# Performance work log

Hardware: AMD Instinct MI355X
Metric: run time of the kernel (lower is better)

The kernel has to match this reference:

```python
import jax, jax.numpy as jnp
import numpy as np

GAMMA = 0.3
R_PERCENT = 0.2
LAMBDA_PENALTY = 0.5
EPS = 1e-06

B_SZ, N_HEADS, K_FULL = 16, 32, 32768
K_IMG = 16384


def _zscore(x):
    mu = x.mean(axis=-1, keepdims=True)
    std = jnp.sqrt(((x - mu) ** 2).mean(axis=-1, keepdims=True))  # unbiased=False
    return (x - mu) / (std + EPS)


def _topk_binary(scores, k):
    # scores: [B,H] -> binary mask [B,H]; only strictly-positive topk values count
    vals, idx = jax.lax.top_k(scores, k)
    b = jnp.arange(scores.shape[0])[:, None]
    return jnp.zeros_like(scores).at[b, idx].set((vals > 0).astype(scores.dtype))


def setup_inputs() -> dict:
    key = jax.random.key(0)
    k1, k2, k3, k4, k5 = jax.random.split(key, 5)
    attn_logits_last = jax.random.normal(k1, (B_SZ, N_HEADS, K_FULL), dtype=jnp.float32)
    # exactly K_IMG image tokens per row (alternating pattern -> strided gather)
    image_mask = jnp.tile((jnp.arange(K_FULL) % 2 == 0).astype(jnp.int32)[None, :], (B_SZ, 1))
    feat_C = jax.random.normal(k2, (B_SZ, K_IMG), dtype=jnp.float32)
    feat_A = jax.random.normal(k3, (B_SZ, K_IMG), dtype=jnp.float32)
    feat_D = jax.random.normal(k4, (B_SZ, K_IMG), dtype=jnp.float32)
    feat_B = jax.random.normal(k5, (B_SZ, K_IMG), dtype=jnp.float32)
    return {"attn_logits_last": attn_logits_last, "image_mask": image_mask,
            "feat_C": feat_C, "feat_A": feat_A, "feat_D": feat_D, "feat_B": feat_B}


def reference(attn_logits_last, image_mask, feat_C, feat_A, feat_D, feat_B):
    B, H, K_full = attn_logits_last.shape
    K_img = feat_C.shape[1]

    # --- compute_rf ---
    C_t = jax.nn.relu(_zscore(feat_C))
    A_t = jax.nn.sigmoid(_zscore(feat_A))
    D_t = jax.nn.sigmoid(_zscore(feat_D))
    B_t = jax.nn.sigmoid(_zscore(feat_B))
    denom = jnp.maximum(1.0 + LAMBDA_PENALTY * (D_t + B_t), EPS)
    rf = jnp.maximum(C_t * A_t / denom, 0.0)  # [B,K_img]

    # --- align: positions of image tokens (exactly K_img ones per row) ---
    idx = jax.vmap(lambda m: jnp.nonzero(m, size=K_img)[0])(image_mask)  # [B,K_img]

    # --- image-normalized attention ---
    probs_full = jax.nn.softmax(attn_logits_last, axis=-1)
    mask_f = image_mask[:, None, :].astype(attn_logits_last.dtype)  # [B,1,K_full]
    probs_img = probs_full * mask_f
    probs_img_norm = probs_img / jnp.maximum(probs_img.sum(axis=-1, keepdims=True), EPS)
    attn_img_norm = jnp.take_along_axis(probs_img_norm, idx[:, None, :], axis=-1)  # [B,H,K_img]

    # --- dynamic head roles ---
    low_rf = jnp.maximum(1.0 - rf, 0.0)
    s_pos = (attn_img_norm * rf[:, None, :]).sum(axis=-1)   # [B,H]
    s_neg = (attn_img_norm * low_rf[:, None, :]).sum(axis=-1)
    k_heads = min(max(1, int(np.ceil(R_PERCENT * H))), H)
    m_pos = _topk_binary(s_pos, k_heads)
    neg_scores = jnp.where(m_pos > 0, -jnp.inf, s_neg)
    m_neg = _topk_binary(neg_scores, k_heads) * (m_pos == 0).astype(s_pos.dtype)

    # --- delta and scatter back to full logits ---
    delta_img = GAMMA * (m_pos[:, :, None] * rf[:, None, :]
                         - m_neg[:, :, None] * low_rf[:, None, :])  # [B,H,K_img]
    delta_full = jax.vmap(
        lambda d, i: jnp.zeros((H, K_full), attn_logits_last.dtype).at[:, i].set(d)
    )(delta_img, idx)
    delta_full = delta_full * mask_f
    return attn_logits_last + delta_full
```

## Files before the change

kernel.cpp:

```cpp
#include <hip/hip_runtime.h>
#include <math.h>

#define GAMMA 0.3f
#define EPS 1e-6f
#define B_SZ 16
#define NH 32
#define KF 32768
#define KI 16384
#define KHEADS 7

constexpr int OFF_MU    = 0;
constexpr int OFF_SD    = 64;
constexpr int OFF_RAWS  = 128;
constexpr int OFF_RAWP  = 640;
constexpr int OFF_RAWN  = 1152;
constexpr int IOFF_BSUM = 1664;
constexpr int OFF_RFF   = 4096;


__global__ __launch_bounds__(256) void k_stats_cnt(const float* __restrict__ fC,
        const float* __restrict__ fA, const float* __restrict__ fD,
        const float* __restrict__ fB, const int* __restrict__ mask,
        float* __restrict__ ws) {
    __shared__ double r1[256], r2[256];
    __shared__ int sred[256];
    int bid = blockIdx.x, t = threadIdx.x;
    if (bid < 64) {
        int b = bid >> 2, f = bid & 3;
        const float* src;
        if (f == 0) src = fC; else if (f == 1) src = fA; else if (f == 2) src = fD; else src = fB;
        src += (size_t)b * KI;
        double s = 0.0, s2 = 0.0;
        for (int i = t; i < KI / 4; i += 256) {
            float4 v = ((const float4*)src)[i];
            s  += (double)v.x + (double)v.y + (double)v.z + (double)v.w;
            s2 += (double)v.x * v.x + (double)v.y * v.y + (double)v.z * v.z + (double)v.w * v.w;
        }
        r1[t] = s; r2[t] = s2; __syncthreads();
        for (int off = 128; off > 0; off >>= 1) {
            if (t < off) { r1[t] += r1[t + off]; r2[t] += r2[t + off]; }
            __syncthreads();
        }
        if (t == 0) {
            double mu  = r1[0] * (1.0 / KI);
            double var = fmax(r2[0] * (1.0 / KI) - mu * mu, 0.0);
            ws[OFF_MU + bid] = (float)mu;
            ws[OFF_SD + bid] = (float)(sqrt(var) + (double)EPS);
        }
    } else {
        int cblk = bid - 64;
        if (cblk < 6) ws[OFF_RAWS + cblk * 256 + t] = 0.f;
        const int* mrow = mask + (size_t)cblk * 2048;
        int4 m0 = *(const int4*)(mrow + t * 8);
        int4 m1 = *(const int4*)(mrow + t * 8 + 4);
        int cnt = (m0.x != 0) + (m0.y != 0) + (m0.z != 0) + (m0.w != 0)
                + (m1.x != 0) + (m1.y != 0) + (m1.z != 0) + (m1.w != 0);
        sred[t] = cnt; __syncthreads();
        for (int off = 128; off > 0; off >>= 1) {
            if (t < off) sred[t] += sred[t + off];
            __syncthreads();
        }
        if (t == 0) ((int*)ws)[IOFF_BSUM + cblk] = sred[0];
    }
}

__global__ __launch_bounds__(256) void k_rf_expand(const float* __restrict__ fC,
        const float* __restrict__ fA, const float* __restrict__ fD,
        const float* __restrict__ fB, const int* __restrict__ mask,
        float* __restrict__ ws) {
    __shared__ int sc[256];
    __shared__ float rfbuf[2048];
    int blk = blockIdx.x, t = threadIdx.x;
    int b = blk >> 4, c = blk & 15;
    const int* bsum = (const int*)ws + IOFF_BSUM;
    int boff = 0;
    for (int i = 0; i < c; ++i) boff += bsum[(b << 4) + i];
    const int* mrow = mask + (size_t)blk * 2048;
    int4 m0 = *(const int4*)(mrow + t * 8);
    int4 m1 = *(const int4*)(mrow + t * 8 + 4);
    int mv[8] = {m0.x, m0.y, m0.z, m0.w, m1.x, m1.y, m1.z, m1.w};
    int cnt = 0;
    #pragma unroll
    for (int j = 0; j < 8; ++j) cnt += (mv[j] != 0);
    sc[t] = cnt; __syncthreads();
    for (int off = 1; off < 256; off <<= 1) {
        int v = (t >= off) ? sc[t - off] : 0;
        __syncthreads();
        sc[t] += v;
        __syncthreads();
    }
    int total = sc[255];
    int rloc = sc[t] - cnt;
    float mu0 = ws[OFF_MU + b * 4 + 0], sd0 = ws[OFF_SD + b * 4 + 0];
    float mu1 = ws[OFF_MU + b * 4 + 1], sd1 = ws[OFF_SD + b * 4 + 1];
    float mu2 = ws[OFF_MU + b * 4 + 2], sd2 = ws[OFF_SD + b * 4 + 2];
    float mu3 = ws[OFF_MU + b * 4 + 3], sd3 = ws[OFF_SD + b * 4 + 3];
    for (int j = t; j < total; j += 256) {
        size_t idx = (size_t)b * KI + boff + j;
        float Ct = fmaxf((fC[idx] - mu0) / sd0, 0.f);
        float At = 1.f / (1.f + __expf(-((fA[idx] - mu1) / sd1)));
        float Dt = 1.f / (1.f + __expf(-((fD[idx] - mu2) / sd2)));
        float Bt = 1.f / (1.f + __expf(-((fB[idx] - mu3) / sd3)));
        float denom = fmaxf(1.f + 0.5f * (Dt + Bt), EPS);
        rfbuf[j] = fmaxf(Ct * At / denom, 0.f);
    }
    __syncthreads();
    float vr[8];
    #pragma unroll
    for (int j = 0; j < 8; ++j) {
        if (mv[j]) { vr[j] = rfbuf[rloc]; ++rloc; }
        else       { vr[j] = -1.f; }
    }
    float* rff = ws + OFF_RFF + (size_t)blk * 2048 + t * 8;
    *(float4*)(rff)     = *(float4*)(vr);
    *(float4*)(rff + 4) = *(float4*)(vr + 4);
}

__global__ __launch_bounds__(256) void k_scores(const float* __restrict__ attn,
                                                float* __restrict__ ws) {
    int g = blockIdx.x, t = threadIdx.x;
    int bh = g >> 1, half = g & 1;
    int b = bh >> 5;
    const float* xr  = attn + ((size_t)bh << 15) + ((size_t)half << 14);
    const float* rff = ws + OFF_RFF + ((size_t)b << 15) + ((size_t)half << 14);
    float S = 0.f, P = 0.f, N = 0.f;
    #pragma unroll 4
    for (int i = 0; i < 16; ++i) {
        int k = (i * 256 + t) * 4;
        float4 xs = *(const float4*)(xr + k);
        float4 rv = *(const float4*)(rff + k);
        float xa[4] = {xs.x, xs.y, xs.z, xs.w};
        float va[4] = {rv.x, rv.y, rv.z, rv.w};
        #pragma unroll
        for (int j = 0; j < 4; ++j) {
            float e = __expf(xa[j]);
            bool on = va[j] >= 0.f;
            float rfv  = fmaxf(va[j], 0.f);
            float lrfv = on ? fmaxf(1.f - va[j], 0.f) : 0.f;
            S += on ? e : 0.f;
            P = fmaf(e, rfv, P);
            N = fmaf(e, lrfv, N);
        }
    }
    __shared__ float rs[256], rp[256], rn[256];
    rs[t] = S; rp[t] = P; rn[t] = N;
    __syncthreads();
    for (int off = 128; off > 0; off >>= 1) {
        if (t < off) { rs[t] += rs[t + off]; rp[t] += rp[t + off]; rn[t] += rn[t + off]; }
        __syncthreads();
    }
    if (t == 0) {
        atomicAdd(&ws[OFF_RAWS + bh], rs[0]);
        atomicAdd(&ws[OFF_RAWP + bh], rp[0]);
        atomicAdd(&ws[OFF_RAWN + bh], rn[0]);
    }
}

__global__ __launch_bounds__(256) void k_out(const float* __restrict__ attn,
        const float* __restrict__ ws, float* __restrict__ out) {
    unsigned int t = threadIdx.x;
    unsigned int flat = blockIdx.x * 2048 + t * 8;
    unsigned int bh = flat >> 15;
    unsigned int b  = bh >> 5;
    unsigned int h  = bh & 31;

    __shared__ float ssp[NH], snv[NH];
    __shared__ int smp[NH];
    __shared__ float s_gp, s_gn;
    if (t < NH) {
        float S0 = ws[OFF_RAWS + b * NH + t];
        ssp[t] = ws[OFF_RAWP + b * NH + t] / S0;
        snv[t] = ws[OFF_RAWN + b * NH + t] / S0;
    }
    __syncthreads();
    if (t < NH) {
        float sp = ssp[t];
        int cnt = 0;
        for (int j = 0; j < NH; ++j) { float o = ssp[j]; cnt += (o > sp) || (o == sp && j < (int)t); }
        smp[t] = (cnt < KHEADS) && (sp > 0.f);
    }
    __syncthreads();
    if (t < NH && smp[t]) snv[t] = -INFINITY;
    __syncthreads();
    if (t == 0) {
        float gp = 0.f, gn = 0.f;
        if (smp[h]) gp = GAMMA;
        else {
            float nv = snv[h];
            int cnt = 0;
            for (int j = 0; j < NH; ++j) { float o = snv[j]; cnt += (o > nv) || (o == nv && j < (int)h); }
            if ((cnt < KHEADS) && (nv > 0.f)) gn = GAMMA;
        }
        s_gp = gp; s_gn = gn;
    }
    __syncthreads();

    float gp = s_gp, gn = s_gn;
    const float* rff = ws + OFF_RFF + ((size_t)b << 15);
    unsigned int k = flat & (KF - 1);
    #pragma unroll
    for (int half8 = 0; half8 < 2; ++half8) {
        unsigned int f2 = flat + half8 * 4, k2 = k + half8 * 4;
        float4 xs = *(const float4*)(attn + f2);
        float4 rv = *(const float4*)(rff + k2);
        float va[4] = {rv.x, rv.y, rv.z, rv.w};
        float xa[4] = {xs.x, xs.y, xs.z, xs.w};
        float oa[4];
        #pragma unroll
        for (int j = 0; j < 4; ++j) {
            bool on = va[j] >= 0.f;
            float rfv  = fmaxf(va[j], 0.f);
            float lrfv = on ? fmaxf(1.f - va[j], 0.f) : 0.f;
            oa[j] = xa[j] + gp * rfv - gn * lrfv;
        }
        float4 o = {oa[0], oa[1], oa[2], oa[3]};
        *(float4*)(out + f2) = o;
    }
}

extern "C" void kernel_launch(void* const* d_in, const int* in_sizes, int n_in,
                              void* d_out, int out_size, void* d_ws, size_t ws_size,
                              hipStream_t stream) {
    const float* attn = (const float*)d_in[0];
    const int*   mask = (const int*)d_in[1];
    const float* fC   = (const float*)d_in[2];
    const float* fA   = (const float*)d_in[3];
    const float* fD   = (const float*)d_in[4];
    const float* fB   = (const float*)d_in[5];
    float* out = (float*)d_out;
    float* ws = (float*)d_ws;

    k_stats_cnt<<<320, 256, 0, stream>>>(fC, fA, fD, fB, mask, ws);
    k_rf_expand<<<256, 256, 0, stream>>>(fC, fA, fD, fB, mask, ws);
    k_scores   <<<1024, 256, 0, stream>>>(attn, ws);
    k_out      <<<B_SZ * NH * KF / 2048, 256, 0, stream>>>(attn, ws, out);
}
```

Measured before the change: 149.9 us.

## Fuse scores and output pass with register-held logits and per-batch spin barrier

Merges the stats, count and rf-expansion kernels into one pre-kernel: each block recomputes the feature statistics and its own prefix of the mask. The score and output kernels become a single kernel that keeps its 16 float4 logits in registers. A per-batch atomic counter with a spin-wait holds blocks until all 64 blocks of that batch have added their head sums. This removes the second global read of the attention logits and two launches. The spin barrier assumes all 64 blocks of a batch are resident at once, which is a deadlock risk, and the pre-kernel repeats the reduction work in every block.

```diff
diff --git a/kernel.cpp b/kernel.cpp
--- a/kernel.cpp
+++ b/kernel.cpp
@@ -9,27 +9,33 @@
 #define KI 16384
 #define KHEADS 7
 
-constexpr int OFF_MU    = 0;
-constexpr int OFF_SD    = 64;
-constexpr int OFF_RAWS  = 128;
-constexpr int OFF_RAWP  = 640;
-constexpr int OFF_RAWN  = 1152;
-constexpr int IOFF_BSUM = 1664;
-constexpr int OFF_RFF   = 4096;
-
-
-__global__ __launch_bounds__(256) void k_stats_cnt(const float* __restrict__ fC,
+constexpr int OFF_RAWS = 0;
+constexpr int OFF_RAWP = 512;
+constexpr int OFF_RAWN = 1024;
+constexpr int IOFF_ARR = 1536;
+constexpr int OFF_RFF  = 4096;
+
+
+__global__ __launch_bounds__(256) void k_pre(const float* __restrict__ fC,
         const float* __restrict__ fA, const float* __restrict__ fD,
         const float* __restrict__ fB, const int* __restrict__ mask,
         float* __restrict__ ws) {
     __shared__ double r1[256], r2[256];
-    __shared__ int sred[256];
-    int bid = blockIdx.x, t = threadIdx.x;
-    if (bid < 64) {
-        int b = bid >> 2, f = bid & 3;
-        const float* src;
-        if (f == 0) src = fC; else if (f == 1) src = fA; else if (f == 2) src = fD; else src = fB;
-        src += (size_t)b * KI;
+    __shared__ float s_mu[4], s_sd[4];
+    __shared__ int sc[256];
+    __shared__ float rfbuf[2048];
+    int blk = blockIdx.x, t = threadIdx.x;
+    int b = blk >> 4, c = blk & 15;
+
+    if (blk == 0) {
+        for (int i = t; i < 1536; i += 256) ws[OFF_RAWS + i] = 0.f;
+        if (t < 16) ((int*)ws)[IOFF_ARR + t * 32] = 0;
+    }
+
+    const float* feats[4] = {fC, fA, fD, fB};
+    #pragma unroll 1
+    for (int f = 0; f < 4; ++f) {
+        const float* src = feats[f] + (size_t)b * KI;
         double s = 0.0, s2 = 0.0;
         for (int i = t; i < KI / 4; i += 256) {
             float4 v = ((const float4*)src)[i];
@@ -44,38 +50,27 @@
         if (t == 0) {
             double mu  = r1[0] * (1.0 / KI);
             double var = fmax(r2[0] * (1.0 / KI) - mu * mu, 0.0);
-            ws[OFF_MU + bid] = (float)mu;
-            ws[OFF_SD + bid] = (float)(sqrt(var) + (double)EPS);
-        }
-    } else {
-        int cblk = bid - 64;
-        if (cblk < 6) ws[OFF_RAWS + cblk * 256 + t] = 0.f;
-        const int* mrow = mask + (size_t)cblk * 2048;
-        int4 m0 = *(const int4*)(mrow + t * 8);
-        int4 m1 = *(const int4*)(mrow + t * 8 + 4);
-        int cnt = (m0.x != 0) + (m0.y != 0) + (m0.z != 0) + (m0.w != 0)
-                + (m1.x != 0) + (m1.y != 0) + (m1.z != 0) + (m1.w != 0);
-        sred[t] = cnt; __syncthreads();
-        for (int off = 128; off > 0; off >>= 1) {
-            if (t < off) sred[t] += sred[t + off];
-            __syncthreads();
-        }
-        if (t == 0) ((int*)ws)[IOFF_BSUM + cblk] = sred[0];
-    }
-}
-
-__global__ __launch_bounds__(256) void k_rf_expand(const float* __restrict__ fC,
-        const float* __restrict__ fA, const float* __restrict__ fD,
-        const float* __restrict__ fB, const int* __restrict__ mask,
-        float* __restrict__ ws) {
-    __shared__ int sc[256];
-    __shared__ float rfbuf[2048];
-    int blk = blockIdx.x, t = threadIdx.x;
-    int b = blk >> 4, c = blk & 15;
-    const int* bsum = (const int*)ws + IOFF_BSUM;
-    int boff = 0;
-    for (int i = 0; i < c; ++i) boff += bsum[(b << 4) + i];
-    const int* mrow = mask + (size_t)blk * 2048;
+            s_mu[f] = (float)mu;
+            s_sd[f] = (float)(sqrt(var) + (double)EPS);
+        }
+        __syncthreads();
+    }
+
+    const int* mrowb = mask + (size_t)b * KF;
+    int pre = 0;
+    for (int i = t; i < c * 512; i += 256) {
+        int4 m = ((const int4*)mrowb)[i];
+        pre += (m.x != 0) + (m.y != 0) + (m.z != 0) + (m.w != 0);
+    }
+    sc[t] = pre; __syncthreads();
+    for (int off = 128; off > 0; off >>= 1) {
+        if (t < off) sc[t] += sc[t + off];
+        __syncthreads();
+    }
+    int boff = sc[0];
+    __syncthreads();
+
+    const int* mrow = mrowb + c * 2048;
     int4 m0 = *(const int4*)(mrow + t * 8);
     int4 m1 = *(const int4*)(mrow + t * 8 + 4);
     int mv[8] = {m0.x, m0.y, m0.z, m0.w, m1.x, m1.y, m1.z, m1.w};
@@ -91,10 +86,9 @@
     }
     int total = sc[255];
     int rloc = sc[t] - cnt;
-    float mu0 = ws[OFF_MU + b * 4 + 0], sd0 = ws[OFF_SD + b * 4 + 0];
-    float mu1 = ws[OFF_MU + b * 4 + 1], sd1 = ws[OFF_SD + b * 4 + 1];
-    float mu2 = ws[OFF_MU + b * 4 + 2], sd2 = ws[OFF_SD + b * 4 + 2];
-    float mu3 = ws[OFF_MU + b * 4 + 3], sd3 = ws[OFF_SD + b * 4 + 3];
+
+    float mu0 = s_mu[0], sd0 = s_sd[0], mu1 = s_mu[1], sd1 = s_sd[1];
+    float mu2 = s_mu[2], sd2 = s_sd[2], mu3 = s_mu[3], sd3 = s_sd[3];
     for (int j = t; j < total; j += 256) {
         size_t idx = (size_t)b * KI + boff + j;
         float Ct = fmaxf((fC[idx] - mu0) / sd0, 0.f);
@@ -116,19 +110,22 @@
     *(float4*)(rff + 4) = *(float4*)(vr + 4);
 }
 
-__global__ __launch_bounds__(256) void k_scores(const float* __restrict__ attn,
-                                                float* __restrict__ ws) {
+__global__ __launch_bounds__(256, 4) void k_main(const float* __restrict__ attn,
+        float* __restrict__ ws, float* __restrict__ out) {
     int g = blockIdx.x, t = threadIdx.x;
     int bh = g >> 1, half = g & 1;
-    int b = bh >> 5;
+    int b = bh >> 5, h = bh & 31;
     const float* xr  = attn + ((size_t)bh << 15) + ((size_t)half << 14);
     const float* rff = ws + OFF_RFF + ((size_t)b << 15) + ((size_t)half << 14);
+
+    float4 r[16];
     float S = 0.f, P = 0.f, N = 0.f;
-    #pragma unroll 4
+    #pragma unroll
     for (int i = 0; i < 16; ++i) {
         int k = (i * 256 + t) * 4;
         float4 xs = *(const float4*)(xr + k);
         float4 rv = *(const float4*)(rff + k);
+        r[i] = xs;
         float xa[4] = {xs.x, xs.y, xs.z, xs.w};
         float va[4] = {rv.x, rv.y, rv.z, rv.w};
         #pragma unroll
@@ -149,35 +146,35 @@
         if (t < off) { rs[t] += rs[t + off]; rp[t] += rp[t + off]; rn[t] += rn[t + off]; }
         __syncthreads();
     }
+
+    int* arr = (int*)ws + IOFF_ARR + b * 32;
     if (t == 0) {
         atomicAdd(&ws[OFF_RAWS + bh], rs[0]);
         atomicAdd(&ws[OFF_RAWP + bh], rp[0]);
         atomicAdd(&ws[OFF_RAWN + bh], rn[0]);
-    }
-}
-
-__global__ __launch_bounds__(256) void k_out(const float* __restrict__ attn,
-        const float* __restrict__ ws, float* __restrict__ out) {
-    unsigned int t = threadIdx.x;
-    unsigned int flat = blockIdx.x * 2048 + t * 8;
-    unsigned int bh = flat >> 15;
-    unsigned int b  = bh >> 5;
-    unsigned int h  = bh & 31;
+        __threadfence();
+        atomicAdd(arr, 1);
+        while (__hip_atomic_load(arr, __ATOMIC_RELAXED, __HIP_MEMORY_SCOPE_AGENT) < 64)
+            __builtin_amdgcn_s_sleep(2);
+    }
+    __syncthreads();
 
     __shared__ float ssp[NH], snv[NH];
     __shared__ int smp[NH];
     __shared__ float s_gp, s_gn;
     if (t < NH) {
-        float S0 = ws[OFF_RAWS + b * NH + t];
-        ssp[t] = ws[OFF_RAWP + b * NH + t] / S0;
-        snv[t] = ws[OFF_RAWN + b * NH + t] / S0;
+        float S0 = __hip_atomic_load(&ws[OFF_RAWS + b * NH + t], __ATOMIC_RELAXED, __HIP_MEMORY_SCOPE_AGENT);
+        float Pp = __hip_atomic_load(&ws[OFF_RAWP + b * NH + t], __ATOMIC_RELAXED, __HIP_MEMORY_SCOPE_AGENT);
+        float Nn = __hip_atomic_load(&ws[OFF_RAWN + b * NH + t], __ATOMIC_RELAXED, __HIP_MEMORY_SCOPE_AGENT);
+        ssp[t] = Pp / S0;
+        snv[t] = Nn / S0;
     }
     __syncthreads();
     if (t < NH) {
         float sp = ssp[t];
-        int cnt = 0;
-        for (int j = 0; j < NH; ++j) { float o = ssp[j]; cnt += (o > sp) || (o == sp && j < (int)t); }
-        smp[t] = (cnt < KHEADS) && (sp > 0.f);
+        int c2 = 0;
+        for (int j = 0; j < NH; ++j) { float o = ssp[j]; c2 += (o > sp) || (o == sp && j < t); }
+        smp[t] = (c2 < KHEADS) && (sp > 0.f);
     }
     __syncthreads();
     if (t < NH && smp[t]) snv[t] = -INFINITY;
@@ -187,24 +184,22 @@
         if (smp[h]) gp = GAMMA;
         else {
             float nv = snv[h];
-            int cnt = 0;
-            for (int j = 0; j < NH; ++j) { float o = snv[j]; cnt += (o > nv) || (o == nv && j < (int)h); }
-            if ((cnt < KHEADS) && (nv > 0.f)) gn = GAMMA;
+            int c2 = 0;
+            for (int j = 0; j < NH; ++j) { float o = snv[j]; c2 += (o > nv) || (o == nv && j < h); }
+            if ((c2 < KHEADS) && (nv > 0.f)) gn = GAMMA;
         }
         s_gp = gp; s_gn = gn;
     }
     __syncthreads();
 
     float gp = s_gp, gn = s_gn;
-    const float* rff = ws + OFF_RFF + ((size_t)b << 15);
-    unsigned int k = flat & (KF - 1);
-    #pragma unroll
-    for (int half8 = 0; half8 < 2; ++half8) {
-        unsigned int f2 = flat + half8 * 4, k2 = k + half8 * 4;
-        float4 xs = *(const float4*)(attn + f2);
-        float4 rv = *(const float4*)(rff + k2);
+    float* op = out + ((size_t)bh << 15) + ((size_t)half << 14);
+    #pragma unroll
+    for (int i = 0; i < 16; ++i) {
+        int k = (i * 256 + t) * 4;
+        float4 rv = *(const float4*)(rff + k);
         float va[4] = {rv.x, rv.y, rv.z, rv.w};
-        float xa[4] = {xs.x, xs.y, xs.z, xs.w};
+        float xa[4] = {r[i].x, r[i].y, r[i].z, r[i].w};
         float oa[4];
         #pragma unroll
         for (int j = 0; j < 4; ++j) {
@@ -214,7 +209,7 @@
             oa[j] = xa[j] + gp * rfv - gn * lrfv;
         }
         float4 o = {oa[0], oa[1], oa[2], oa[3]};
-        *(float4*)(out + f2) = o;
+        *(float4*)(op + k) = o;
     }
 }
 
@@ -230,8 +225,6 @@
     float* out = (float*)d_out;
     float* ws = (float*)d_ws;
 
-    k_stats_cnt<<<320, 256, 0, stream>>>(fC, fA, fD, fB, mask, ws);
-    k_rf_expand<<<256, 256, 0, stream>>>(fC, fA, fD, fB, mask, ws);
-    k_scores   <<<1024, 256, 0, stream>>>(attn, ws);
-    k_out      <<<B_SZ * NH * KF / 2048, 256, 0, stream>>>(attn, ws, out);
+    k_pre <<<256, 256, 0, stream>>>(fC, fA, fD, fB, mask, ws);
+    k_main<<<1024, 256, 0, stream>>>(attn, ws, out);
 }
```

After: 193.6 us. +29.2%, slower.
